# Performance work log

Hardware: AMD Instinct MI355X
Metric: run time of the kernel (lower is better)

## Reference

```python
import math
import jax, jax.numpy as jnp
import numpy as np

EMBED_DIM = 1024
NUM_HEADS = 16
HEAD_DIM = EMBED_DIM // NUM_HEADS
NUM_BUCKETS = 32
MAX_DISTANCE = 128


def _relative_position_bucket(relative_position, num_buckets=NUM_BUCKETS, max_distance=MAX_DISTANCE):
    # Bidirectional T5 bucketing (matches torch reference exactly).
    num_buckets = num_buckets // 2
    relative_buckets = (relative_position > 0).astype(jnp.int32) * num_buckets
    relative_position = jnp.abs(relative_position)
    max_exact = num_buckets // 2
    is_small = relative_position < max_exact
    rp_large = jnp.log(relative_position.astype(jnp.float32) / max_exact) / math.log(max_distance / max_exact)
    rp_large = max_exact + (rp_large * (num_buckets - max_exact)).astype(jnp.int32)
    rp_large = jnp.minimum(rp_large, num_buckets - 1)
    relative_buckets = relative_buckets + jnp.where(is_small, relative_position, rp_large)
    return relative_buckets


def compute_bias(rel_emb, query_length, key_length):
    context_position = jnp.arange(query_length, dtype=jnp.int32)[:, None]
    memory_position = jnp.arange(key_length, dtype=jnp.int32)[None, :]
    relative_position = memory_position - context_position  # [q, k]
    buckets = _relative_position_bucket(relative_position)
    values = rel_emb[buckets]                 # [q, k, h]
    return jnp.transpose(values, (2, 0, 1))[None]  # [1, h, q, k]


def setup_inputs() -> dict:
    key = jax.random.key(0)
    k1, k2, k3, k4 = jax.random.split(key, 4)
    B, S = 2, 2048
    hidden_states = jax.random.normal(k1, (B, S, EMBED_DIM), dtype=jnp.float32)
    scale = 1.0 / math.sqrt(EMBED_DIM)
    W_qkv = jax.random.normal(k2, (EMBED_DIM, 3 * EMBED_DIM), dtype=jnp.float32) * scale
    W_out = jax.random.normal(k3, (EMBED_DIM, EMBED_DIM), dtype=jnp.float32) * scale
    rel_emb = jax.random.normal(k4, (NUM_BUCKETS, NUM_HEADS), dtype=jnp.float32) * 0.02
    return {"hidden_states": hidden_states, "W_qkv": W_qkv, "W_out": W_out, "rel_emb": rel_emb}


def reference(hidden_states, W_qkv, W_out, rel_emb):
    B, S, _ = hidden_states.shape
    qkv = hidden_states @ W_qkv                                # [B, S, 3*D]
    qkv = qkv.reshape(B, S, 3, NUM_HEADS, HEAD_DIM)
    qkv = jnp.transpose(qkv, (0, 3, 2, 1, 4))                  # [B, H, 3, S, dh]
    q, k, v = qkv[:, :, 0], qkv[:, :, 1], qkv[:, :, 2]
    scores = jnp.einsum('bhqd,bhkd->bhqk', q, k)               # no 1/sqrt(d) scaling (T5 style)
    scores = scores + compute_bias(rel_emb, S, S)
    attn = jax.nn.softmax(scores.astype(jnp.float32), axis=-1).astype(scores.dtype)
    out = jnp.einsum('bhqk,bhkd->bhqd', attn, v)               # [B, H, S, dh]
    out = jnp.transpose(out, (0, 2, 1, 3)).reshape(B, S, EMBED_DIM)
    return out @ W_out
```

## Files before the change

### kernel.cpp

```cpp
#include <hip/hip_runtime.h>
#include <hip/hip_bf16.h>
#include <math.h>

typedef _Float16 f16;
typedef __attribute__((ext_vector_type(8))) _Float16 f16x8;
typedef __attribute__((ext_vector_type(4))) _Float16 f16x4;
typedef __attribute__((ext_vector_type(4))) float f32x4;

#define EMBED 1024
#define NHEADS 16
#define HDIM 64
#define BATCH 2
#define SEQ 2048
#define BS 4096
#define LOG2E 1.4426950408889634f


__device__ __forceinline__ f32x4 mfma16x32(f16x8 a, f16x8 b, f32x4 c) {
  return __builtin_amdgcn_mfma_f32_16x16x32_f16(a, b, c, 0, 0, 0);
}
__device__ __forceinline__ f32x4 mfma16x16(f16x4 a, f16x4 b, f32x4 c) {
  return __builtin_amdgcn_mfma_f32_16x16x16f16(a, b, c, 0, 0, 0);
}
__device__ __forceinline__ void gload_lds16(const f16* __restrict__ g, f16* l) {
  __builtin_amdgcn_global_load_lds(
      (const __attribute__((address_space(1))) void*)g,
      (__attribute__((address_space(3))) void*)l, 16, 0, 0);
}

__global__ void prep_kernel(const float* __restrict__ X, const float* __restrict__ Wqkv,
                            const float* __restrict__ Wout, const float* __restrict__ rel_emb,
                            f16* __restrict__ Xh, f16* __restrict__ Wqkv_t,
                            f16* __restrict__ Wout_t, float* __restrict__ btab) {
  __shared__ float tile[32][33];
  int bid = blockIdx.x, tid = threadIdx.x;
  if (bid < 4096) {
    int i = (bid * 256 + tid) * 4;
    float4 v = *(const float4*)(X + i);
    f16x4 o = { (f16)v.x, (f16)v.y, (f16)v.z, (f16)v.w };
    *(f16x4*)(Xh + i) = o;
  } else if (bid < 8192) {
    const float* in;
    f16* out;
    int N, idx;
    if (bid < 7168) { in = Wqkv; out = Wqkv_t; N = 3072; idx = bid - 4096; }
    else            { in = Wout; out = Wout_t; N = 1024; idx = bid - 7168; }
    int nt = N / 32;
    int n0 = (idx % nt) * 32, k0 = (idx / nt) * 32;
    int tx = tid & 31, ty = tid >> 5;
#pragma unroll
    for (int r = ty; r < 32; r += 8) tile[r][tx] = in[(size_t)(k0 + r) * N + n0 + tx];
    __syncthreads();
#pragma unroll
    for (int r = ty; r < 32; r += 8) out[(size_t)(n0 + r) * 1024 + k0 + tx] = (f16)tile[tx][r];
  } else {
    int idx = (bid - 8192) * 256 + tid;
    if (idx >= 4095) return;
    int rp = idx - 2047;
    int rb = rp > 0 ? 16 : 0;
    int arp = rp < 0 ? -rp : rp;
    int loc;
    if (arp < 8) {
      loc = arp;
    } else {
      float lr = logf((float)arp * 0.125f) * (1.0f / 2.7725887222397811f);
      int t = 8 + (int)(lr * 8.0f);
      loc = t < 15 ? t : 15;
    }
    int bucket = rb + loc;
#pragma unroll
    for (int h = 0; h < 16; h++) btab[h * 4095 + idx] = rel_emb[bucket * 16 + h] * LOG2E;
  }
}

__device__ __forceinline__ void gemm_core(const f16* __restrict__ A, const f16* __restrict__ Bt,
                                          int m0, int n0, int Kdim, f32x4 (&acc)[4][4]) {
  __shared__ __align__(16) f16 As[128 * 32];
  __shared__ __align__(16) f16 Bs[128 * 32];

  int tid = threadIdx.x;
  int lane = tid & 63, wave = tid >> 6;
  int l15 = lane & 15, quad = lane >> 4;
  int wr = (wave >> 1) * 64, wc = (wave & 1) * 64;
  int rowl = lane >> 2;
  int col8 = (lane & 3) * 8;

#pragma unroll
  for (int i = 0; i < 4; i++)
#pragma unroll
    for (int j = 0; j < 4; j++) acc[i][j] = f32x4{0.f, 0.f, 0.f, 0.f};

  for (int kt = 0; kt < Kdim / 32; kt++) {
    int kk = kt * 32;
#pragma unroll
    for (int c = 0; c < 2; c++) {
      int row = wave * 32 + c * 16 + rowl;
      gload_lds16(A + (size_t)(m0 + row) * Kdim + kk + col8, &As[(wave * 32 + c * 16) * 32]);
      gload_lds16(Bt + (size_t)(n0 + row) * Kdim + kk + col8, &Bs[(wave * 32 + c * 16) * 32]);
    }
    __syncthreads();
    f16x8 af[4], bf[4];
#pragma unroll
    for (int i = 0; i < 4; i++) af[i] = *(const f16x8*)(&As[(wr + i * 16 + l15) * 32 + quad * 8]);
#pragma unroll
    for (int j = 0; j < 4; j++) bf[j] = *(const f16x8*)(&Bs[(wc + j * 16 + l15) * 32 + quad * 8]);
#pragma unroll
    for (int i = 0; i < 4; i++)
#pragma unroll
      for (int j = 0; j < 4; j++) acc[i][j] = mfma16x32(af[i], bf[j], acc[i][j]);
    __syncthreads();
  }
}

__global__ __launch_bounds__(256, 2) void gemm_qkv_kernel(
    const f16* __restrict__ Xh, const f16* __restrict__ Wt,
    f16* __restrict__ Q, f16* __restrict__ K_, f16* __restrict__ Vp) {
  f32x4 acc[4][4];
  int m0 = blockIdx.y * 128, n0 = blockIdx.x * 128;
  gemm_core(Xh, Wt, m0, n0, 1024, acc);

  int lane = threadIdx.x & 63, wave = threadIdx.x >> 6;
  int l15 = lane & 15, quad = lane >> 4;
  int wr = (wave >> 1) * 64, wc = (wave & 1) * 64;
  int nq = n0 + wc;
  int which = nq >> 10;
  int h = (nq >> 6) & 15;
  int b = m0 >> 11;

  if (which == 2) {
    int s0 = (m0 & 2047) + wr;
    f16* vbase = Vp + (size_t)(b * 16 + h) * 131072 + (size_t)(s0 >> 6) * 4096;
#pragma unroll
    for (int i = 0; i < 4; i++) {
#pragma unroll
      for (int jp = 0; jp < 2; jp++) {
        f16x8 pk = { (f16)acc[i][2 * jp][0],     (f16)acc[i][2 * jp][1],
                     (f16)acc[i][2 * jp][2],     (f16)acc[i][2 * jp][3],
                     (f16)acc[i][2 * jp + 1][0], (f16)acc[i][2 * jp + 1][1],
                     (f16)acc[i][2 * jp + 1][2], (f16)acc[i][2 * jp + 1][3] };
        *(f16x8*)(vbase + (i * 2 + jp) * 512 + lane * 8) = pk;
      }
    }
  } else {
    f16* base = (which == 0) ? Q : K_;
    float sc = (which == 0) ? LOG2E : 1.0f;
#pragma unroll
    for (int i = 0; i < 4; i++) {
#pragma unroll
      for (int j = 0; j < 4; j++) {
        int d = j * 16 + l15;
#pragma unroll
        for (int r = 0; r < 4; r++) {
          int m = m0 + wr + i * 16 + quad * 4 + r;
          int s = m & 2047;
          base[(((size_t)(b * 16 + h) * 2048 + s) << 6) + d] = (f16)(acc[i][j][r] * sc);
        }
      }
    }
  }
}

__global__ void repack_k_kernel(const f16* __restrict__ Kw, f16* __restrict__ Kp) {
  int o = blockIdx.x * 256 + threadIdx.x;
  int lane = o & 63;
  int ct = (o >> 6) & 7;
  int kt = (o >> 9) & 31;
  int bh = o >> 14;
  int c = ct >> 1, t = ct & 1;
  int l15 = lane & 15, quad = lane >> 4;
  int s = kt * 64 + c * 16 + l15;
  f16x8 v = *(const f16x8*)(Kw + ((size_t)(bh * 2048 + s) << 6) + t * 32 + quad * 8);
  *(f16x8*)(Kp + (size_t)o * 8) = v;
}

__global__ __launch_bounds__(256, 4) void attn_kernel(
    const f16* __restrict__ Q, const f16* __restrict__ Kp, const f16* __restrict__ Vp,
    const float* __restrict__ btab, f16* __restrict__ O) {
  __shared__ float bias_lds[2112];

  int qt = blockIdx.x, bh = blockIdx.y;
  int qbase = qt * 64;
  int h = bh & 15, b = bh >> 4;
  int tid = threadIdx.x, lane = tid & 63, wave = tid >> 6;
  int l15 = lane & 15, quad = lane >> 4;

  const float* brow = btab + h * 4095 + (1984 - qbase);
  for (int i = tid; i < 2111; i += 256) bias_lds[i] = brow[i];

  const f16* qptr = Q + ((size_t)bh * 2048 + qbase + wave * 16 + l15) * 64 + quad * 8;
  f16x8 qf0 = *(const f16x8*)(qptr);
  f16x8 qf1 = *(const f16x8*)(qptr + 32);

  f32x4 accO[4] = {};
  float m_i = -INFINITY, l_i = 0.f;

  const f16* kc = Kp + (size_t)bh * 131072 + 1792;
  const f16* vc = Vp + (size_t)bh * 131072 + 1792;
  const int voff = lane * 8;
  const int bofs = quad * 4 - wave * 16 - l15 + 63;

  __syncthreads();

  for (int kt = 0; kt < 32; kt++) {
    const float* bb = &bias_lds[kt * 64 + bofs];
    f32x4 scT[4];
#pragma unroll
    for (int c = 0; c < 4; c++) {
      scT[c] = f32x4{ bb[c * 16], bb[c * 16 + 1], bb[c * 16 + 2], bb[c * 16 + 3] };
      f16x8 kf0 = *(const f16x8*)(kc + ((c * 2 + 0) * 512 - 1792) + voff);
      f16x8 kf1 = *(const f16x8*)(kc + ((c * 2 + 1) * 512 - 1792) + voff);
      scT[c] = mfma16x32(kf0, qf0, scT[c]);
      scT[c] = mfma16x32(kf1, qf1, scT[c]);
    }
    f16x8 vf8[4][2];
#pragma unroll
    for (int c = 0; c < 4; c++)
#pragma unroll
      for (int jp = 0; jp < 2; jp++)
        vf8[c][jp] = *(const f16x8*)(vc + ((c * 2 + jp) * 512 - 1792) + voff);
    float mp0 = fmaxf(fmaxf(scT[0][0], scT[0][1]), fmaxf(scT[0][2], scT[0][3]));
    float mp1 = fmaxf(fmaxf(scT[1][0], scT[1][1]), fmaxf(scT[1][2], scT[1][3]));
    float mp2 = fmaxf(fmaxf(scT[2][0], scT[2][1]), fmaxf(scT[2][2], scT[2][3]));
    float mp3 = fmaxf(fmaxf(scT[3][0], scT[3][1]), fmaxf(scT[3][2], scT[3][3]));
    float mp = fmaxf(fmaxf(mp0, mp1), fmaxf(mp2, mp3));
    if (__any(mp > m_i)) {
      float mx = fmaxf(mp, __shfl_xor(mp, 16));
      mx = fmaxf(mx, __shfl_xor(mx, 32));
      float mn = fmaxf(m_i, mx);
      float alpha = exp2f(m_i - mn);
      m_i = mn;
      l_i *= alpha;
      float arow[4];
#pragma unroll
      for (int r = 0; r < 4; r++) arow[r] = __shfl(alpha, quad * 4 + r);
#pragma unroll
      for (int d = 0; d < 4; d++)
#pragma unroll
        for (int r = 0; r < 4; r++) accO[d][r] *= arow[r];
    }
    float mx = m_i;
    f16x4 p[4];
    float rc[4];
#pragma unroll
    for (int c = 0; c < 4; c++) {
      float e0 = exp2f(scT[c][0] - mx);
      float e1 = exp2f(scT[c][1] - mx);
      float e2 = exp2f(scT[c][2] - mx);
      float e3 = exp2f(scT[c][3] - mx);
      rc[c] = (e0 + e1) + (e2 + e3);
      p[c][0] = (f16)e0; p[c][1] = (f16)e1; p[c][2] = (f16)e2; p[c][3] = (f16)e3;
    }
    float rs = (rc[0] + rc[1]) + (rc[2] + rc[3]);
    rs += __shfl_xor(rs, 16);
    rs += __shfl_xor(rs, 32);
    l_i += rs;
#pragma unroll
    for (int c = 0; c < 4; c++) {
#pragma unroll
      for (int jp = 0; jp < 2; jp++) {
        f16x4 vlo = __builtin_shufflevector(vf8[c][jp], vf8[c][jp], 0, 1, 2, 3);
        f16x4 vhi = __builtin_shufflevector(vf8[c][jp], vf8[c][jp], 4, 5, 6, 7);
        accO[2 * jp]     = mfma16x16(p[c], vlo, accO[2 * jp]);
        accO[2 * jp + 1] = mfma16x16(p[c], vhi, accO[2 * jp + 1]);
      }
    }
    kc += 4096;
    vc += 4096;
  }

  float linv = 1.0f / l_i;
  float lrow[4];
#pragma unroll
  for (int r = 0; r < 4; r++) lrow[r] = __shfl(linv, quad * 4 + r);
#pragma unroll
  for (int dblk = 0; dblk < 4; dblk++) {
#pragma unroll
    for (int r = 0; r < 4; r++) {
      int q = qbase + wave * 16 + quad * 4 + r;
      O[((size_t)(b * 2048 + q) << 10) + h * 64 + dblk * 16 + l15] = (f16)(accO[dblk][r] * lrow[r]);
    }
  }
}

__global__ __launch_bounds__(256, 2) void gemm_out_kernel(
    const f16* __restrict__ Oh, const f16* __restrict__ Wt, float* __restrict__ out) {
  f32x4 acc[4][4];
  int m0 = blockIdx.y * 128, n0 = blockIdx.x * 128;
  gemm_core(Oh, Wt, m0, n0, 1024, acc);

  int lane = threadIdx.x & 63, wave = threadIdx.x >> 6;
  int l15 = lane & 15, quad = lane >> 4;
  int wr = (wave >> 1) * 64, wc = (wave & 1) * 64;
#pragma unroll
  for (int i = 0; i < 4; i++) {
#pragma unroll
    for (int j = 0; j < 4; j++) {
      int n = n0 + wc + j * 16 + l15;
#pragma unroll
      for (int r = 0; r < 4; r++) {
        int m = m0 + wr + i * 16 + quad * 4 + r;
        out[((size_t)m << 10) + n] = acc[i][j][r];
      }
    }
  }
}

extern "C" void kernel_launch(void* const* d_in, const int* in_sizes, int n_in,
                              void* d_out, int out_size, void* d_ws, size_t ws_size,
                              hipStream_t stream) {
  const float* X = (const float*)d_in[0];
  const float* Wqkv = (const float*)d_in[1];
  const float* Wout = (const float*)d_in[2];
  const float* rel = (const float*)d_in[3];

  char* ws = (char*)d_ws;
  f16* Xh     = (f16*)(ws + 0);
  f16* Kp     = (f16*)(ws + 0);
  f16* Wqkv_t = (f16*)(ws + 8388608);
  f16* Wout_t = (f16*)(ws + 14680064);
  f16* Qw     = (f16*)(ws + 16777216);
  f16* Kw     = (f16*)(ws + 25165824);
  f16* Vp     = (f16*)(ws + 33554432);
  f16* Ow     = (f16*)(ws + 41943040);
  float* btab = (float*)(ws + 50331648);

  prep_kernel<<<8208, 256, 0, stream>>>(X, Wqkv, Wout, rel, Xh, Wqkv_t, Wout_t, btab);
  gemm_qkv_kernel<<<dim3(24, 32), 256, 0, stream>>>(Xh, Wqkv_t, Qw, Kw, Vp);
  repack_k_kernel<<<2048, 256, 0, stream>>>(Kw, Kp);
  attn_kernel<<<dim3(32, 32), 256, 0, stream>>>(Qw, Kp, Vp, btab, Ow);
  gemm_out_kernel<<<dim3(8, 32), 256, 0, stream>>>(Ow, Wout_t, (float*)d_out);
}
```

Baseline: 223.6 us.

## Shrink output GEMM tile to 128x64, pack softmax converts, raise QKV occupancy

The output projection GEMM now uses its own 128x64 tile (each wave computes a 32x64 slice) instead of the shared 128x128 core. This doubles the grid from 256 to 512 blocks so the 256 CUs of the MI355X have more than one block each. In the attention softmax, the four scalar f16 conversions are replaced with packed round-toward-zero conversions (cvt_pkrtz), which changes the rounding mode. The QKV GEMM launch bounds also ask for three blocks per CU instead of two, which may force register spills.

```diff
diff --git a/kernel.cpp b/kernel.cpp
--- a/kernel.cpp
+++ b/kernel.cpp
@@ -5,6 +5,7 @@
 typedef _Float16 f16;
 typedef __attribute__((ext_vector_type(8))) _Float16 f16x8;
 typedef __attribute__((ext_vector_type(4))) _Float16 f16x4;
+typedef __attribute__((ext_vector_type(2))) _Float16 f16x2;
 typedef __attribute__((ext_vector_type(4))) float f32x4;
 
 #define EMBED 1024
@@ -21,6 +22,9 @@
 }
 __device__ __forceinline__ f32x4 mfma16x16(f16x4 a, f16x4 b, f32x4 c) {
   return __builtin_amdgcn_mfma_f32_16x16x16f16(a, b, c, 0, 0, 0);
+}
+__device__ __forceinline__ f16x2 cvt_pk(float a, float b) {
+  return __builtin_bit_cast(f16x2, __builtin_amdgcn_cvt_pkrtz(a, b));
 }
 __device__ __forceinline__ void gload_lds16(const f16* __restrict__ g, f16* l) {
   __builtin_amdgcn_global_load_lds(
@@ -112,7 +116,7 @@
   }
 }
 
-__global__ __launch_bounds__(256, 2) void gemm_qkv_kernel(
+__global__ __launch_bounds__(256, 3) void gemm_qkv_kernel(
     const f16* __restrict__ Xh, const f16* __restrict__ Wt,
     f16* __restrict__ Q, f16* __restrict__ K_, f16* __restrict__ Vp) {
   f32x4 acc[4][4];
@@ -248,7 +252,9 @@
       float e2 = exp2f(scT[c][2] - mx);
       float e3 = exp2f(scT[c][3] - mx);
       rc[c] = (e0 + e1) + (e2 + e3);
-      p[c][0] = (f16)e0; p[c][1] = (f16)e1; p[c][2] = (f16)e2; p[c][3] = (f16)e3;
+      f16x2 plo = cvt_pk(e0, e1);
+      f16x2 phi = cvt_pk(e2, e3);
+      p[c][0] = plo[0]; p[c][1] = plo[1]; p[c][2] = phi[0]; p[c][3] = phi[1];
     }
     float rs = (rc[0] + rc[1]) + (rc[2] + rc[3]);
     rs += __shfl_xor(rs, 16);
@@ -284,18 +290,52 @@
 
 __global__ __launch_bounds__(256, 2) void gemm_out_kernel(
     const f16* __restrict__ Oh, const f16* __restrict__ Wt, float* __restrict__ out) {
-  f32x4 acc[4][4];
-  int m0 = blockIdx.y * 128, n0 = blockIdx.x * 128;
-  gemm_core(Oh, Wt, m0, n0, 1024, acc);
-
-  int lane = threadIdx.x & 63, wave = threadIdx.x >> 6;
-  int l15 = lane & 15, quad = lane >> 4;
-  int wr = (wave >> 1) * 64, wc = (wave & 1) * 64;
-#pragma unroll
-  for (int i = 0; i < 4; i++) {
+  __shared__ __align__(16) f16 As[128 * 32];
+  __shared__ __align__(16) f16 Bs[64 * 32];
+
+  int tid = threadIdx.x;
+  int lane = tid & 63, wave = tid >> 6;
+  int l15 = lane & 15, quad = lane >> 4;
+  int rowl = lane >> 2;
+  int col8 = (lane & 3) * 8;
+  int m0 = blockIdx.y * 128, n0 = blockIdx.x * 64;
+  int wr = wave * 32;
+
+  f32x4 acc[2][4];
+#pragma unroll
+  for (int i = 0; i < 2; i++)
+#pragma unroll
+    for (int j = 0; j < 4; j++) acc[i][j] = f32x4{0.f, 0.f, 0.f, 0.f};
+
+  for (int kt = 0; kt < 32; kt++) {
+    int kk = kt * 32;
+#pragma unroll
+    for (int c = 0; c < 2; c++) {
+      int row = wave * 32 + c * 16 + rowl;
+      gload_lds16(Oh + (size_t)(m0 + row) * 1024 + kk + col8, &As[(wave * 32 + c * 16) * 32]);
+    }
+    {
+      int row = wave * 16 + rowl;
+      gload_lds16(Wt + (size_t)(n0 + row) * 1024 + kk + col8, &Bs[(wave * 16) * 32]);
+    }
+    __syncthreads();
+    f16x8 af[2], bf[4];
+#pragma unroll
+    for (int i = 0; i < 2; i++) af[i] = *(const f16x8*)(&As[(wr + i * 16 + l15) * 32 + quad * 8]);
+#pragma unroll
+    for (int j = 0; j < 4; j++) bf[j] = *(const f16x8*)(&Bs[(j * 16 + l15) * 32 + quad * 8]);
+#pragma unroll
+    for (int i = 0; i < 2; i++)
+#pragma unroll
+      for (int j = 0; j < 4; j++) acc[i][j] = mfma16x32(af[i], bf[j], acc[i][j]);
+    __syncthreads();
+  }
+
+#pragma unroll
+  for (int i = 0; i < 2; i++) {
 #pragma unroll
     for (int j = 0; j < 4; j++) {
-      int n = n0 + wc + j * 16 + l15;
+      int n = n0 + j * 16 + l15;
 #pragma unroll
       for (int r = 0; r < 4; r++) {
         int m = m0 + wr + i * 16 + quad * 4 + r;
@@ -328,5 +368,5 @@
   gemm_qkv_kernel<<<dim3(24, 32), 256, 0, stream>>>(Xh, Wqkv_t, Qw, Kw, Vp);
   repack_k_kernel<<<2048, 256, 0, stream>>>(Kw, Kp);
   attn_kernel<<<dim3(32, 32), 256, 0, stream>>>(Qw, Kp, Vp, btab, Ow);
-  gemm_out_kernel<<<dim3(8, 32), 256, 0, stream>>>(Ow, Wout_t, (float*)d_out);
-}
+  gemm_out_kernel<<<dim3(16, 32), 256, 0, stream>>>(Ow, Wout_t, (float*)d_out);
+}
```

Measured after the change: 224.9 us. About the same (+0.6%).
